# Performance work log

Measured on AMD Instinct MI355X. Metric: run time of the kernel, lower is better.

The kernel has to match this reference:

```python
import jax, jax.numpy as jnp
import numpy as np

B, K, F, HID, NCLS = 32, 32, 2048, 2, 47
BN_EPS = 1e-5


def setup_inputs() -> dict:
    key = jax.random.key(0)
    ks = jax.random.split(key, 12)
    x = jax.random.normal(ks[0], (B, 1, F), dtype=jnp.float32)
    neighbor = jax.random.normal(ks[1], (B, K, 1, F), dtype=jnp.float32)
    # FeatBrd1d conv1d kernel_size=1 weights: (out_ch, in_ch)
    w1 = jax.random.normal(ks[2], (HID, 1), dtype=jnp.float32) * 0.5
    b1 = jax.random.normal(ks[3], (HID,), dtype=jnp.float32) * 0.1
    g1 = jnp.ones((HID,), dtype=jnp.float32)
    beta1 = jnp.zeros((HID,), dtype=jnp.float32)
    w2 = jax.random.normal(ks[4], (HID, HID), dtype=jnp.float32) * 0.5
    b2 = jax.random.normal(ks[5], (HID,), dtype=jnp.float32) * 0.1
    g2 = jnp.ones((HID,), dtype=jnp.float32)
    beta2 = jnp.zeros((HID,), dtype=jnp.float32)
    Wc = jax.random.normal(ks[6], (NCLS, HID * F), dtype=jnp.float32) * (1.0 / np.sqrt(HID * F))
    bc = jnp.zeros((NCLS,), dtype=jnp.float32)
    return {"x": x, "neighbor": neighbor, "w1": w1, "b1": b1, "g1": g1,
            "beta1": beta1, "w2": w2, "b2": b2, "g2": g2, "beta2": beta2,
            "Wc": Wc, "bc": bc}


def feature_adjacency(x, neighbor):
    # fadj[b] = sum_{k} x[b,0,:] outer neighbor[b,k,0,:]  -> (B, F, F)
    ysum = neighbor.sum(axis=(1, 2))                      # (B, F)
    fadj = jnp.einsum('bf,bg->bfg', x[:, 0, :], ysum)
    fadj = fadj + jnp.swapaxes(fadj, -2, -1)
    # sgnroot
    fadj = jnp.sign(fadj) * jnp.sqrt(jnp.abs(fadj))
    # row_normalize (torch sums over dim=1 of (B,F,F))
    denom = jnp.abs(fadj).sum(axis=1, keepdims=True) + 1e-7
    fadj = fadj / denom
    return jnp.nan_to_num(fadj, nan=0.0, posinf=None, neginf=None)


def featbrd(x, fadj, w, b):
    # conv1d kernel-size-1: (B, Cin, F) x (Cout, Cin) -> (B, Cout, F)
    h = jnp.einsum('bif,oi->bof', x, w) + b[None, :, None]
    # adj broadcast: out[b,c,f] = sum_g fadj[b,f,g] * h[b,c,g]
    return jnp.einsum('bfg,bcg->bcf', fadj, h)


def bn_softsign(x, gamma, beta):
    # BatchNorm1d training mode over (B, C, F): stats per channel over (B, F)
    mean = x.mean(axis=(0, 2), keepdims=True)
    var = ((x - mean) ** 2).mean(axis=(0, 2), keepdims=True)
    xn = (x - mean) * jax.lax.rsqrt(var + BN_EPS)
    y = gamma[None, :, None] * xn + beta[None, :, None]
    return y / (1.0 + jnp.abs(y))  # Softsign


def reference(x, neighbor, w1, b1, g1, beta1, w2, b2, g2, beta2, Wc, bc):
    fadj = feature_adjacency(x, neighbor)
    h = bn_softsign(featbrd(x, fadj, w1, b1), g1, beta1)
    h = bn_softsign(featbrd(h, fadj, w2, b2), g2, beta2)
    flat = h.reshape(h.shape[0], -1)                      # (B, HID*F)
    return flat @ Wc.T + bc
```

## Files before the change

### kernel.cpp

```cpp
#include <hip/hip_runtime.h>
#include <math.h>

namespace {

constexpr int Bn   = 32;
constexpr int Kn   = 32;
constexpr int Fn   = 2048;
constexpr int HIDn = 2;
constexpr int NCLSn = 47;
constexpr float EPSn = 1e-5f;
constexpr int NT = 256;
constexpr int GS = 32;
constexpr int FT = Fn / GS;

typedef float v2f __attribute__((ext_vector_type(2)));
typedef float v4f __attribute__((ext_vector_type(4)));

__device__ inline float wave_sum(float v) {
    #pragma unroll
    for (int off = 32; off > 0; off >>= 1) v += __shfl_down(v, off, 64);
    return v;
}

__global__ void ysum_kernel(const float* __restrict__ neighbor,
                            float* __restrict__ ysum,
                            double* __restrict__ stats) {
    int idx4 = blockIdx.x * NT + threadIdx.x;
    if (blockIdx.x == 0 && threadIdx.x < 8) stats[threadIdx.x] = 0.0;
    int b = idx4 >> 9;
    int gq = idx4 & 511;
    const float* p = neighbor + (size_t)b * Kn * Fn + gq * 4;
    v4f s = (v4f){0.f, 0.f, 0.f, 0.f};
    #pragma unroll
    for (int k = 0; k < Kn; ++k) s += *(const v4f*)(p + (size_t)k * Fn);
    *(v4f*)(ysum + (size_t)b * Fn + gq * 4) = s;
}

__global__ __launch_bounds__(NT, 8)
void denom_partial_kernel(const float* __restrict__ x, const float* __restrict__ ysum,
                          float* __restrict__ dpart) {
    __shared__ v2f xf2[FT], yf2[FT];
    const int gtile = blockIdx.x;
    const int fs    = blockIdx.y;
    const int b     = blockIdx.z;
    const int tid   = threadIdx.x;
    const float* xb = x + (size_t)b * Fn;
    const float* yb = ysum + (size_t)b * Fn;
    if (tid < FT) {
        int f = fs * FT + tid;
        float xv = xb[f], yv = yb[f];
        xf2[tid] = (v2f){xv, xv};
        yf2[tid] = (v2f){yv, yv};
    }
    const int gbase = (gtile * NT + tid) * 4;
    const v4f Xg4 = *(const v4f*)(xb + gbase);
    const v4f Yg4 = *(const v4f*)(yb + gbase);
    const v2f Xg01 = (v2f){Xg4.x, Xg4.y}, Xg23 = (v2f){Xg4.z, Xg4.w};
    const v2f Yg01 = (v2f){Yg4.x, Yg4.y}, Yg23 = (v2f){Yg4.z, Yg4.w};
    __syncthreads();
    v2f d01 = (v2f){0.f, 0.f}, d23 = (v2f){0.f, 0.f};
    #pragma unroll 4
    for (int j = 0; j < FT; ++j) {
        v2f xf = xf2[j], yf = yf2[j];
        v2f vA = Xg01 * yf + Yg01 * xf;
        v2f vB = Xg23 * yf + Yg23 * xf;
        v2f sA, sB;
        sA.x = __builtin_amdgcn_sqrtf(fabsf(vA.x));
        sA.y = __builtin_amdgcn_sqrtf(fabsf(vA.y));
        sB.x = __builtin_amdgcn_sqrtf(fabsf(vB.x));
        sB.y = __builtin_amdgcn_sqrtf(fabsf(vB.y));
        d01 += sA;
        d23 += sB;
    }
    v4f dout = (v4f){d01.x, d01.y, d23.x, d23.y};
    *(v4f*)(dpart + ((size_t)fs * Bn + b) * Fn + gbase) = dout;
}

__device__ inline void mv_loop4(const v2f* __restrict__ xg2, const v2f* __restrict__ yg2,
                                const v2f* __restrict__ t02, const v2f* __restrict__ t12,
                                v2f Xf01, v2f Xf23, v2f Yf01, v2f Yf23,
                                v2f& a00, v2f& a10, v2f& a01, v2f& a11) {
    #pragma unroll 4
    for (int j = 0; j < FT; ++j) {
        v2f xg = xg2[j], yg = yg2[j];
        v2f vA = Xf01 * yg + Yf01 * xg;
        v2f vB = Xf23 * yg + Yf23 * xg;
        v2f SA, SB;
        SA.x = copysignf(__builtin_amdgcn_sqrtf(fabsf(vA.x)), vA.x);
        SA.y = copysignf(__builtin_amdgcn_sqrtf(fabsf(vA.y)), vA.y);
        SB.x = copysignf(__builtin_amdgcn_sqrtf(fabsf(vB.x)), vB.x);
        SB.y = copysignf(__builtin_amdgcn_sqrtf(fabsf(vB.y)), vB.y);
        v2f t0 = t02[j], t1 = t12[j];
        a00 += SA * t0;
        a10 += SA * t1;
        a01 += SB * t0;
        a11 += SB * t1;
    }
}

__global__ __launch_bounds__(NT, 8)
void mv1_partial_kernel(const float* __restrict__ x, const float* __restrict__ ysum,
                        const float* __restrict__ dpart,
                        const float* __restrict__ w1, const float* __restrict__ b1,
                        float* __restrict__ part) {
    __shared__ v2f xg2[FT], yg2[FT], t02[FT], t12[FT];
    const int ftile = blockIdx.x;
    const int gs    = blockIdx.y;
    const int b     = blockIdx.z;
    const int tid   = threadIdx.x;
    const float* xb = x + (size_t)b * Fn;
    const float* yb = ysum + (size_t)b * Fn;
    if (tid < FT) {
        int g = gs * FT + tid;
        float d = 0.f;
        #pragma unroll
        for (int fs = 0; fs < GS; ++fs) d += dpart[((size_t)fs * Bn + b) * Fn + g];
        float r = 1.0f / (d + 1e-7f);
        float xg = xb[g], yg = yb[g];
        float t0 = fmaf(w1[0], xg, b1[0]) * r;
        float t1 = fmaf(w1[1], xg, b1[1]) * r;
        xg2[tid] = (v2f){xg, xg};
        yg2[tid] = (v2f){yg, yg};
        t02[tid] = (v2f){t0, t0};
        t12[tid] = (v2f){t1, t1};
    }
    const int fbase = (ftile * NT + tid) * 4;
    const v4f X4 = *(const v4f*)(xb + fbase);
    const v4f Y4 = *(const v4f*)(yb + fbase);
    __syncthreads();
    v2f a00 = (v2f){0.f, 0.f}, a10 = a00, a01 = a00, a11 = a00;
    mv_loop4(xg2, yg2, t02, t12,
             (v2f){X4.x, X4.y}, (v2f){X4.z, X4.w},
             (v2f){Y4.x, Y4.y}, (v2f){Y4.z, Y4.w}, a00, a10, a01, a11);
    size_t base = (((size_t)gs * Bn + b) * HIDn) * Fn;
    *(v4f*)(part + base + fbase)      = (v4f){a00.x, a00.y, a01.x, a01.y};
    *(v4f*)(part + base + Fn + fbase) = (v4f){a10.x, a10.y, a11.x, a11.y};
}

__global__ __launch_bounds__(NT, 8)
void mv2_partial_kernel(const float* __restrict__ x, const float* __restrict__ ysum,
                        const float* __restrict__ dpart, const float* __restrict__ out1,
                        const double* __restrict__ stats,
                        const float* __restrict__ g1, const float* __restrict__ beta1,
                        const float* __restrict__ w2, const float* __restrict__ b2,
                        float* __restrict__ part) {
    __shared__ v2f xg2[FT], yg2[FT], t02[FT], t12[FT];
    const int ftile = blockIdx.x;
    const int gs    = blockIdx.y;
    const int b     = blockIdx.z;
    const int tid   = threadIdx.x;
    const float* xb = x + (size_t)b * Fn;
    const float* yb = ysum + (size_t)b * Fn;
    if (tid < FT) {
        const double N = (double)(Bn * Fn);
        double m0d = stats[0] / N, m1d = stats[1] / N;
        float mean0 = (float)m0d, mean1 = (float)m1d;
        float var0 = (float)(stats[2] / N - m0d * m0d);
        float var1 = (float)(stats[3] / N - m1d * m1d);
        float inv0 = rsqrtf(var0 + EPSn) * g1[0];
        float inv1 = rsqrtf(var1 + EPSn) * g1[1];
        int g = gs * FT + tid;
        float d = 0.f;
        #pragma unroll
        for (int fs = 0; fs < GS; ++fs) d += dpart[((size_t)fs * Bn + b) * Fn + g];
        float r = 1.0f / (d + 1e-7f);
        size_t obase = ((size_t)b * HIDn) * Fn + g;
        float o0 = out1[obase], o1 = out1[obase + Fn];
        float y0 = fmaf(o0 - mean0, inv0, beta1[0]);
        float y1 = fmaf(o1 - mean1, inv1, beta1[1]);
        float z0 = y0 / (1.f + fabsf(y0));
        float z1 = y1 / (1.f + fabsf(y1));
        float t0 = fmaf(w2[0], z0, fmaf(w2[1], z1, b2[0])) * r;
        float t1 = fmaf(w2[2], z0, fmaf(w2[3], z1, b2[1])) * r;
        float xg = xb[g], yg = yb[g];
        xg2[tid] = (v2f){xg, xg};
        yg2[tid] = (v2f){yg, yg};
        t02[tid] = (v2f){t0, t0};
        t12[tid] = (v2f){t1, t1};
    }
    const int fbase = (ftile * NT + tid) * 4;
    const v4f X4 = *(const v4f*)(xb + fbase);
    const v4f Y4 = *(const v4f*)(yb + fbase);
    __syncthreads();
    v2f a00 = (v2f){0.f, 0.f}, a10 = a00, a01 = a00, a11 = a00;
    mv_loop4(xg2, yg2, t02, t12,
             (v2f){X4.x, X4.y}, (v2f){X4.z, X4.w},
             (v2f){Y4.x, Y4.y}, (v2f){Y4.z, Y4.w}, a00, a10, a01, a11);
    size_t base = (((size_t)gs * Bn + b) * HIDn) * Fn;
    *(v4f*)(part + base + fbase)      = (v4f){a00.x, a00.y, a01.x, a01.y};
    *(v4f*)(part + base + Fn + fbase) = (v4f){a10.x, a10.y, a11.x, a11.y};
}

__global__ void mv_reduce_kernel(const float* __restrict__ part, float* __restrict__ out,
                                 double* __restrict__ stats) {
    __shared__ float red[4][4];
    int pidx = blockIdx.x * NT + threadIdx.x;
    int b = pidx >> 9;
    int fq = pidx & 511;
    const size_t stride = (size_t)Bn * HIDn * Fn;
    size_t base = ((size_t)b * HIDn) * Fn + fq * 4;
    v4f o0 = (v4f){0.f, 0.f, 0.f, 0.f}, o1 = o0;
    #pragma unroll
    for (int gs = 0; gs < GS; ++gs) {
        o0 += *(const v4f*)(part + (size_t)gs * stride + base);
        o1 += *(const v4f*)(part + (size_t)gs * stride + base + Fn);
    }
    *(v4f*)(out + base)      = o0;
    *(v4f*)(out + base + Fn) = o1;
    float s0 = wave_sum((o0.x + o0.y) + (o0.z + o0.w));
    float s1 = wave_sum((o1.x + o1.y) + (o1.z + o1.w));
    float q0 = wave_sum((o0.x * o0.x + o0.y * o0.y) + (o0.z * o0.z + o0.w * o0.w));
    float q1 = wave_sum((o1.x * o1.x + o1.y * o1.y) + (o1.z * o1.z + o1.w * o1.w));
    int wid = threadIdx.x >> 6, lane = threadIdx.x & 63;
    if (lane == 0) { red[wid][0] = s0; red[wid][1] = s1; red[wid][2] = q0; red[wid][3] = q1; }
    __syncthreads();
    if (threadIdx.x == 0) {
        double S0 = 0, S1 = 0, Q0 = 0, Q1 = 0;
        #pragma unroll
        for (int w = 0; w < 4; ++w) {
            S0 += red[w][0]; S1 += red[w][1]; Q0 += red[w][2]; Q1 += red[w][3];
        }
        atomicAdd(&stats[0], S0);
        atomicAdd(&stats[1], S1);
        atomicAdd(&stats[2], Q0);
        atomicAdd(&stats[3], Q1);
    }
}

__global__ void classifier_kernel(const float* __restrict__ out2, const double* __restrict__ stats,
                                  const float* __restrict__ g2, const float* __restrict__ beta2,
                                  const float* __restrict__ Wc, const float* __restrict__ bc,
                                  float* __restrict__ out) {
    __shared__ float z[HIDn * Fn];
    const int n = blockIdx.x;
    const int b = blockIdx.y;
    const double N = (double)(Bn * Fn);
    double m0d = stats[0] / N, m1d = stats[1] / N;
    float mean0 = (float)m0d, mean1 = (float)m1d;
    float var0 = (float)(stats[2] / N - m0d * m0d);
    float var1 = (float)(stats[3] / N - m1d * m1d);
    float inv0 = rsqrtf(var0 + EPSn) * g2[0];
    float inv1 = rsqrtf(var1 + EPSn) * g2[1];
    float bet0 = beta2[0], bet1 = beta2[1];
    const float* src = out2 + (size_t)b * HIDn * Fn;
    #pragma unroll
    for (int it = 0; it < (HIDn * Fn) / NT; ++it) {
        int i = it * NT + threadIdx.x;
        int c = i >> 11;
        float v = src[i];
        float y = fmaf(v - (c ? mean1 : mean0), (c ? inv1 : inv0), (c ? bet1 : bet0));
        z[i] = y / (1.f + fabsf(y));
    }
    __syncthreads();
    const float4* z4 = (const float4*)z;
    const float4* w4 = (const float4*)(Wc + (size_t)n * (HIDn * Fn));
    float acc = 0.f;
    #pragma unroll
    for (int it = 0; it < (HIDn * Fn) / (4 * NT); ++it) {
        int i = it * NT + threadIdx.x;
        float4 a = z4[i];
        float4 w = w4[i];
        acc = fmaf(a.x, w.x, acc);
        acc = fmaf(a.y, w.y, acc);
        acc = fmaf(a.z, w.z, acc);
        acc = fmaf(a.w, w.w, acc);
    }
    __shared__ float red[4];
    float s = wave_sum(acc);
    int wid = threadIdx.x >> 6, lane = threadIdx.x & 63;
    if (lane == 0) red[wid] = s;
    __syncthreads();
    if (threadIdx.x == 0) {
        float tot = (red[0] + red[1]) + (red[2] + red[3]);
        out[(size_t)b * NCLSn + n] = tot + bc[n];
    }
}

}

extern "C" void kernel_launch(void* const* d_in, const int* in_sizes, int n_in,
                              void* d_out, int out_size, void* d_ws, size_t ws_size,
                              hipStream_t stream) {
    const float* x        = (const float*)d_in[0];
    const float* neighbor = (const float*)d_in[1];
    const float* w1       = (const float*)d_in[2];
    const float* b1       = (const float*)d_in[3];
    const float* g1       = (const float*)d_in[4];
    const float* beta1    = (const float*)d_in[5];
    const float* w2       = (const float*)d_in[6];
    const float* b2       = (const float*)d_in[7];
    const float* g2       = (const float*)d_in[8];
    const float* beta2    = (const float*)d_in[9];
    const float* Wc       = (const float*)d_in[10];
    const float* bc       = (const float*)d_in[11];
    float* out = (float*)d_out;

    float* ws    = (float*)d_ws;
    float* ysum  = ws;
    float* dpart = ysum + Bn * Fn;
    float* part  = dpart + (size_t)GS * Bn * Fn;
    float* out1  = part + (size_t)GS * Bn * HIDn * Fn;
    float* out2  = out1 + Bn * HIDn * Fn;
    double* stats = (double*)(out2 + Bn * HIDn * Fn);

    const dim3 grid_split(Fn / (NT * 4), GS, Bn);

    ysum_kernel<<<(Bn * Fn / 4) / NT, NT, 0, stream>>>(neighbor, ysum, stats);
    denom_partial_kernel<<<grid_split, NT, 0, stream>>>(x, ysum, dpart);
    mv1_partial_kernel<<<grid_split, NT, 0, stream>>>(x, ysum, dpart, w1, b1, part);
    mv_reduce_kernel<<<(Bn * Fn / 4) / NT, NT, 0, stream>>>(part, out1, stats);
    mv2_partial_kernel<<<grid_split, NT, 0, stream>>>(x, ysum, dpart, out1, stats, g1, beta1, w2, b2, part);
    mv_reduce_kernel<<<(Bn * Fn / 4) / NT, NT, 0, stream>>>(part, out2, stats + 4);
    classifier_kernel<<<dim3(NCLSn, Bn), NT, 0, stream>>>(out2, stats + 4, g2, beta2, Wc, bc, out);
}
```

Baseline: 98.85 us.

## Halve split count, pack shared operands into float4, deepen unroll

Reduces the number of g-splits from 32 to 16, so each block loops over twice as many columns. This halves the partial buffers and the reduction work, at the cost of fewer blocks and lower launch-bound occupancy. Shared-memory operands are packed into interleaved float4 arrays so each iteration does one wide LDS read instead of two. The inner-loop unroll is raised from 4 to 8.

```diff
diff --git a/kernel.cpp b/kernel.cpp
--- a/kernel.cpp
+++ b/kernel.cpp
@@ -10,7 +10,7 @@
 constexpr int NCLSn = 47;
 constexpr float EPSn = 1e-5f;
 constexpr int NT = 256;
-constexpr int GS = 32;
+constexpr int GS = 16;
 constexpr int FT = Fn / GS;
 
 typedef float v2f __attribute__((ext_vector_type(2)));
@@ -36,10 +36,10 @@
     *(v4f*)(ysum + (size_t)b * Fn + gq * 4) = s;
 }
 
-__global__ __launch_bounds__(NT, 8)
+__global__ __launch_bounds__(NT, 4)
 void denom_partial_kernel(const float* __restrict__ x, const float* __restrict__ ysum,
                           float* __restrict__ dpart) {
-    __shared__ v2f xf2[FT], yf2[FT];
+    __shared__ v4f xyf4[FT];
     const int gtile = blockIdx.x;
     const int fs    = blockIdx.y;
     const int b     = blockIdx.z;
@@ -49,8 +49,7 @@
     if (tid < FT) {
         int f = fs * FT + tid;
         float xv = xb[f], yv = yb[f];
-        xf2[tid] = (v2f){xv, xv};
-        yf2[tid] = (v2f){yv, yv};
+        xyf4[tid] = (v4f){xv, xv, yv, yv};
     }
     const int gbase = (gtile * NT + tid) * 4;
     const v4f Xg4 = *(const v4f*)(xb + gbase);
@@ -59,9 +58,10 @@
     const v2f Yg01 = (v2f){Yg4.x, Yg4.y}, Yg23 = (v2f){Yg4.z, Yg4.w};
     __syncthreads();
     v2f d01 = (v2f){0.f, 0.f}, d23 = (v2f){0.f, 0.f};
-    #pragma unroll 4
+    #pragma unroll 8
     for (int j = 0; j < FT; ++j) {
-        v2f xf = xf2[j], yf = yf2[j];
+        v4f q = xyf4[j];
+        v2f xf = (v2f){q.x, q.y}, yf = (v2f){q.z, q.w};
         v2f vA = Xg01 * yf + Yg01 * xf;
         v2f vB = Xg23 * yf + Yg23 * xf;
         v2f sA, sB;
@@ -76,13 +76,13 @@
     *(v4f*)(dpart + ((size_t)fs * Bn + b) * Fn + gbase) = dout;
 }
 
-__device__ inline void mv_loop4(const v2f* __restrict__ xg2, const v2f* __restrict__ yg2,
-                                const v2f* __restrict__ t02, const v2f* __restrict__ t12,
+__device__ inline void mv_loop4(const v4f* __restrict__ xy4, const v4f* __restrict__ tt4,
                                 v2f Xf01, v2f Xf23, v2f Yf01, v2f Yf23,
                                 v2f& a00, v2f& a10, v2f& a01, v2f& a11) {
-    #pragma unroll 4
+    #pragma unroll 8
     for (int j = 0; j < FT; ++j) {
-        v2f xg = xg2[j], yg = yg2[j];
+        v4f q = xy4[j];
+        v2f xg = (v2f){q.x, q.y}, yg = (v2f){q.z, q.w};
         v2f vA = Xf01 * yg + Yf01 * xg;
         v2f vB = Xf23 * yg + Yf23 * xg;
         v2f SA, SB;
@@ -90,7 +90,8 @@
         SA.y = copysignf(__builtin_amdgcn_sqrtf(fabsf(vA.y)), vA.y);
         SB.x = copysignf(__builtin_amdgcn_sqrtf(fabsf(vB.x)), vB.x);
         SB.y = copysignf(__builtin_amdgcn_sqrtf(fabsf(vB.y)), vB.y);
-        v2f t0 = t02[j], t1 = t12[j];
+        v4f u = tt4[j];
+        v2f t0 = (v2f){u.x, u.y}, t1 = (v2f){u.z, u.w};
         a00 += SA * t0;
         a10 += SA * t1;
         a01 += SB * t0;
@@ -98,12 +99,12 @@
     }
 }
 
-__global__ __launch_bounds__(NT, 8)
+__global__ __launch_bounds__(NT, 4)
 void mv1_partial_kernel(const float* __restrict__ x, const float* __restrict__ ysum,
                         const float* __restrict__ dpart,
                         const float* __restrict__ w1, const float* __restrict__ b1,
                         float* __restrict__ part) {
-    __shared__ v2f xg2[FT], yg2[FT], t02[FT], t12[FT];
+    __shared__ v4f xy4[FT], tt4[FT];
     const int ftile = blockIdx.x;
     const int gs    = blockIdx.y;
     const int b     = blockIdx.z;
@@ -119,17 +120,15 @@
         float xg = xb[g], yg = yb[g];
         float t0 = fmaf(w1[0], xg, b1[0]) * r;
         float t1 = fmaf(w1[1], xg, b1[1]) * r;
-        xg2[tid] = (v2f){xg, xg};
-        yg2[tid] = (v2f){yg, yg};
-        t02[tid] = (v2f){t0, t0};
-        t12[tid] = (v2f){t1, t1};
+        xy4[tid] = (v4f){xg, xg, yg, yg};
+        tt4[tid] = (v4f){t0, t0, t1, t1};
     }
     const int fbase = (ftile * NT + tid) * 4;
     const v4f X4 = *(const v4f*)(xb + fbase);
     const v4f Y4 = *(const v4f*)(yb + fbase);
     __syncthreads();
     v2f a00 = (v2f){0.f, 0.f}, a10 = a00, a01 = a00, a11 = a00;
-    mv_loop4(xg2, yg2, t02, t12,
+    mv_loop4(xy4, tt4,
              (v2f){X4.x, X4.y}, (v2f){X4.z, X4.w},
              (v2f){Y4.x, Y4.y}, (v2f){Y4.z, Y4.w}, a00, a10, a01, a11);
     size_t base = (((size_t)gs * Bn + b) * HIDn) * Fn;
@@ -137,14 +136,14 @@
     *(v4f*)(part + base + Fn + fbase) = (v4f){a10.x, a10.y, a11.x, a11.y};
 }
 
-__global__ __launch_bounds__(NT, 8)
+__global__ __launch_bounds__(NT, 4)
 void mv2_partial_kernel(const float* __restrict__ x, const float* __restrict__ ysum,
                         const float* __restrict__ dpart, const float* __restrict__ out1,
                         const double* __restrict__ stats,
                         const float* __restrict__ g1, const float* __restrict__ beta1,
                         const float* __restrict__ w2, const float* __restrict__ b2,
                         float* __restrict__ part) {
-    __shared__ v2f xg2[FT], yg2[FT], t02[FT], t12[FT];
+    __shared__ v4f xy4[FT], tt4[FT];
     const int ftile = blockIdx.x;
     const int gs    = blockIdx.y;
     const int b     = blockIdx.z;
@@ -173,17 +172,15 @@
         float t0 = fmaf(w2[0], z0, fmaf(w2[1], z1, b2[0])) * r;
         float t1 = fmaf(w2[2], z0, fmaf(w2[3], z1, b2[1])) * r;
         float xg = xb[g], yg = yb[g];
-        xg2[tid] = (v2f){xg, xg};
-        yg2[tid] = (v2f){yg, yg};
-        t02[tid] = (v2f){t0, t0};
-        t12[tid] = (v2f){t1, t1};
+        xy4[tid] = (v4f){xg, xg, yg, yg};
+        tt4[tid] = (v4f){t0, t0, t1, t1};
     }
     const int fbase = (ftile * NT + tid) * 4;
     const v4f X4 = *(const v4f*)(xb + fbase);
     const v4f Y4 = *(const v4f*)(yb + fbase);
     __syncthreads();
     v2f a00 = (v2f){0.f, 0.f}, a10 = a00, a01 = a00, a11 = a00;
-    mv_loop4(xg2, yg2, t02, t12,
+    mv_loop4(xy4, tt4,
              (v2f){X4.x, X4.y}, (v2f){X4.z, X4.w},
              (v2f){Y4.x, Y4.y}, (v2f){Y4.z, Y4.w}, a00, a10, a01, a11);
     size_t base = (((size_t)gs * Bn + b) * HIDn) * Fn;
```

Measured after the change: 92.96 us, median of 2. -6.0%, faster.
